# Optimization experiments

Hardware: AMD Instinct MI355X
Metric: run time of the kernel (lower is better)

## Reference

```python
import jax, jax.numpy as jnp
import numpy as np

N, H, V, K = 2048, 1024, 50304, 16
C = V // K  # tokens per POS cluster


def setup_inputs() -> dict:
    key = jax.random.key(0)
    kx, ky, kw, kl = jax.random.split(key, 4)
    x = jax.random.normal(kx, (N, H), dtype=jnp.float32)
    y = jax.random.randint(ky, (N,), 0, V, dtype=jnp.int32)
    # consistent POS label: token y belongs to cluster y // C
    y_pos = (y // C).astype(jnp.int32)
    # pos2token[i] = token ids of cluster i (equal contiguous partition)
    pos2token = jnp.arange(V, dtype=jnp.int32).reshape(K, C)
    # token_in_pos_id[i][v] = within-cluster index of token v in cluster i
    token_in_pos_id = jnp.broadcast_to(jnp.arange(V, dtype=jnp.int32) % C, (K, V))
    cluster_w = jax.random.normal(kw, (H, K), dtype=jnp.float32) * 0.02
    logits = jax.random.normal(kl, (H, V), dtype=jnp.float32) * 0.02
    return {"x": x, "y": y, "y_pos": y_pos, "pos2token": pos2token,
            "token_in_pos_id": token_in_pos_id, "cluster_w": cluster_w, "logits": logits}


def reference(x, y, y_pos, pos2token, token_in_pos_id, cluster_w, logits):
    # cluster (POS) log-probs: [N, K]
    cluster_ll = jax.nn.log_softmax(x @ cluster_w, axis=1)
    # per-cluster weight slices gathered once: [H, K, C]
    W = logits[:, pos2token.reshape(-1)].reshape(H, K, C)
    # tail logits for every token against every cluster's token set: [N, K, C]
    tail_lp = jax.nn.log_softmax(jnp.einsum('nh,hkc->nkc', x, W), axis=-1)
    n = jnp.arange(y.shape[0])
    within = token_in_pos_id[y_pos, y]          # within-cluster target id
    nll = -cluster_ll[n, y_pos] - tail_lp[n, y_pos, within]
    return nll
```

## Files before the change

kernel.cpp:

```cpp
#include <hip/hip_runtime.h>
#include <hip/hip_bf16.h>
#include <stdint.h>

#define NROW 2048
#define HDIM 1024
#define VOC  50304
#define KCL  16
#define CDIM 3144

#define MT 64
#define NT 128
#define BK 32
#define MAXTILES 48

#define WS_SUMEXP 0
#define WS_COUNTS 2048
#define WS_PART   2064
#define WS_ZTGT   4112
#define WS_TCOL   6160
#define WS_ROWS   8208
#define WS_NTILE  40976
#define WS_TILES  40977
#define WS_XB     65536
#define WS_BT     (65536 + 1048576)

typedef unsigned short u16;
typedef __attribute__((ext_vector_type(8))) short short8;
typedef __attribute__((ext_vector_type(4))) float f32x4;
typedef __attribute__((ext_vector_type(4))) unsigned short ushort4v;
typedef __attribute__((ext_vector_type(8))) unsigned short ushort8v;

__device__ __forceinline__ ushort2 f2bf2(float a, float b) {
    union { __hip_bfloat162 h; ushort2 u; } cv;
    cv.h = __float22bfloat162_rn(float2{a, b});
    return cv.u;
}

__device__ __forceinline__ void gload16(const void* g, void* lds) {
    __builtin_amdgcn_global_load_lds(
        (__attribute__((address_space(1))) void*)(g),
        (__attribute__((address_space(3))) void*)(lds), 16, 0, 0);
}

__global__ void scatter_kernel(const int* __restrict__ y,
                               const int* __restrict__ y_pos,
                               const int* __restrict__ tip,
                               int* ws_i) {
    int n = blockIdx.x * 256 + threadIdx.x;
    if (n >= NROW) return;
    int kn = y_pos[n];
    int slot = atomicAdd(&ws_i[WS_COUNTS + kn], 1);
    ws_i[WS_ROWS + kn * NROW + slot] = n;
    ws_i[WS_TCOL + n] = tip[kn * VOC + y[n]];
}

__global__ void plan_kernel(int* ws_i) {
    if (threadIdx.x == 0) {
        int t = 0;
        for (int k = 0; k < KCL; k++) {
            int mk = ws_i[WS_COUNTS + k];
            int nt = (mk + MT - 1) / MT;
            for (int r = 0; r < nt; r++) {
                ws_i[WS_TILES + 2 * t]     = k;
                ws_i[WS_TILES + 2 * t + 1] = r;
                t++;
            }
        }
        ws_i[WS_NTILE] = t;
    }
}

__global__ void cluster_kernel(const float* __restrict__ x,
                               const float* __restrict__ cw,
                               const int* __restrict__ y_pos,
                               float* ws_f) {
    int wave = threadIdx.x >> 6;
    int lane = threadIdx.x & 63;
    int n = blockIdx.x * 4 + wave;
    float acc[KCL];
#pragma unroll
    for (int k = 0; k < KCL; k++) acc[k] = 0.f;
#pragma unroll
    for (int j = 0; j < 16; j++) {
        int h = j * 64 + lane;
        float xv = x[(size_t)n * HDIM + h];
        const float4* cwr = (const float4*)(cw + (size_t)h * KCL);
#pragma unroll
        for (int q = 0; q < 4; q++) {
            float4 w = cwr[q];
            acc[q * 4 + 0] += xv * w.x;
            acc[q * 4 + 1] += xv * w.y;
            acc[q * 4 + 2] += xv * w.z;
            acc[q * 4 + 3] += xv * w.w;
        }
    }
#pragma unroll
    for (int off = 32; off >= 1; off >>= 1) {
#pragma unroll
        for (int k = 0; k < KCL; k++) acc[k] += __shfl_down(acc[k], off);
    }
    if (lane == 0) {
        int kn = y_pos[n];
        float m = acc[0];
#pragma unroll
        for (int k = 1; k < KCL; k++) m = fmaxf(m, acc[k]);
        float s = 0.f, skn = 0.f;
#pragma unroll
        for (int k = 0; k < KCL; k++) {
            s += __expf(acc[k] - m);
            skn = (k == kn) ? acc[k] : skn;
        }
        ws_f[WS_PART + n] = (m + __logf(s)) - skn;
    }
}

__global__ void convx_kernel(const float* __restrict__ x, u16* __restrict__ xb) {
    int t = blockIdx.x * 256 + threadIdx.x;
    float4 f = ((const float4*)x)[t];
    ushort2 a = f2bf2(f.x, f.y);
    ushort2 b = f2bf2(f.z, f.w);
    ushort4v v = {a.x, a.y, b.x, b.y};
    *(ushort4v*)(xb + (size_t)t * 4) = v;
}

#define TV 128
#define TH 128
#define THP 136
__global__ void transpose_kernel(const float* __restrict__ L, u16* __restrict__ Bt) {
    __shared__ u16 Ls[TV * THP];
    const int v0 = blockIdx.x * TV;
    const int h0 = blockIdx.y * TH;
    const int t  = threadIdx.x;
    {
        const int vi = (t & 31) * 4;
        const int hi = t >> 5;
#pragma unroll
        for (int p = 0; p < 16; p++) {
            int hh = p * 8 + hi;
            float4 f = *(const float4*)(L + (size_t)(h0 + hh) * VOC + v0 + vi);
            ushort2 u01 = f2bf2(f.x, f.y);
            ushort2 u23 = f2bf2(f.z, f.w);
            Ls[(vi + 0) * THP + hh] = u01.x;
            Ls[(vi + 1) * THP + hh] = u01.y;
            Ls[(vi + 2) * THP + hh] = u23.x;
            Ls[(vi + 3) * THP + hh] = u23.y;
        }
    }
    __syncthreads();
    {
        const int hi = (t & 15) * 8;
        const int vi = t >> 4;
#pragma unroll
        for (int p = 0; p < 8; p++) {
            int v = p * 16 + vi;
            ushort8v val = *(const ushort8v*)&Ls[v * THP + hi];
            *(ushort8v*)(Bt + (size_t)(v0 + v) * HDIM + h0 + hi) = val;
        }
    }
}

__launch_bounds__(256, 4)
__global__ void tail_kernel(const u16* __restrict__ xb,
                            const u16* __restrict__ Bt,
                            const int* ws_i, float* ws_f) {
    __shared__ __align__(16) u16 As[MT * BK];
    __shared__ __align__(16) u16 Bs[NT * BK];
    __shared__ int   lrow[MT];
    __shared__ int   ltcol[MT];
    __shared__ float rowsum[MT];

    const int ntile = ws_i[WS_NTILE];
    if ((int)blockIdx.y >= ntile) return;
    const int kcl = ws_i[WS_TILES + 2 * blockIdx.y];
    const int rt  = ws_i[WS_TILES + 2 * blockIdx.y + 1];
    const int ct  = blockIdx.x;
    const int Mk  = ws_i[WS_COUNTS + kcl];

    const int tid = threadIdx.x;
    if (tid < MT) {
        int r = rt * MT + tid;
        int rid = (r < Mk) ? ws_i[WS_ROWS + kcl * NROW + r] : -1;
        lrow[tid]  = rid;
        ltcol[tid] = (rid >= 0) ? ws_i[WS_TCOL + rid] : -1;
        rowsum[tid] = 0.f;
    }
    __syncthreads();

    const int w    = tid >> 6;
    const int l    = tid & 63;
    const int quad = l >> 4;
    const int lm   = l & 15;

    int arow = w * 16 + (l >> 2);
    int rid_s = lrow[arow]; if (rid_s < 0) rid_s = 0;
    const u16* agp = xb + (size_t)rid_s * HDIM + (l & 3) * 8;
    u16* alds = (u16*)As + w * 512;
    int c0 = w * 32 + (l >> 2);
    int c1 = c0 + 16;
    int g0 = ct * NT + c0; if (g0 >= CDIM) g0 = CDIM - 1;
    int g1 = ct * NT + c1; if (g1 >= CDIM) g1 = CDIM - 1;
    const u16* bgp0 = Bt + (size_t)(kcl * CDIM + g0) * HDIM + (l & 3) * 8;
    const u16* bgp1 = Bt + (size_t)(kcl * CDIM + g1) * HDIM + (l & 3) * 8;
    u16* blds0 = (u16*)Bs + w * 1024;
    u16* blds1 = (u16*)Bs + w * 1024 + 512;

    f32x4 acc[4][2];
#pragma unroll
    for (int mi = 0; mi < 4; mi++)
#pragma unroll
        for (int ni = 0; ni < 2; ni++) acc[mi][ni] = (f32x4)(0.f);

    for (int h0 = 0; h0 < HDIM; h0 += BK) {
        gload16(agp, alds);
        gload16(bgp0, blds0);
        gload16(bgp1, blds1);
        agp += BK; bgp0 += BK; bgp1 += BK;
        __syncthreads();

        short8 a[4], b[2];
#pragma unroll
        for (int mi = 0; mi < 4; mi++)
            a[mi] = *(const short8*)&As[(mi * 16 + lm) * BK + quad * 8];
#pragma unroll
        for (int ni = 0; ni < 2; ni++)
            b[ni] = *(const short8*)&Bs[(w * 32 + ni * 16 + lm) * BK + quad * 8];
#pragma unroll
        for (int mi = 0; mi < 4; mi++)
#pragma unroll
            for (int ni = 0; ni < 2; ni++)
                acc[mi][ni] = __builtin_amdgcn_mfma_f32_16x16x32_bf16(
                    a[mi], b[ni], acc[mi][ni], 0, 0, 0);
        __syncthreads();
    }

#pragma unroll
    for (int mi = 0; mi < 4; mi++) {
#pragma unroll
        for (int r = 0; r < 4; r++) {
            int row_local = mi * 16 + quad * 4 + r;
            int rid = lrow[row_local];
            int tc  = ltcol[row_local];
            float s = 0.f;
#pragma unroll
            for (int ni = 0; ni < 2; ni++) {
                int cl = ct * NT + w * 32 + ni * 16 + lm;
                float z = acc[mi][ni][r];
                if (rid >= 0 && cl < CDIM) {
                    s += __expf(z);
                    if (cl == tc) ws_f[WS_ZTGT + rid] = z;
                }
            }
            s += __shfl_xor(s, 1);
            s += __shfl_xor(s, 2);
            s += __shfl_xor(s, 4);
            s += __shfl_xor(s, 8);
            if (lm == 0 && rid >= 0) atomicAdd(&rowsum[row_local], s);
        }
    }
    __syncthreads();
    if (tid < MT) {
        int rid = lrow[tid];
        if (rid >= 0) atomicAdd(&ws_f[WS_SUMEXP + rid], rowsum[tid]);
    }
}

__global__ void finalize_kernel(const float* ws_f, float* __restrict__ out) {
    int n = blockIdx.x * 256 + threadIdx.x;
    if (n >= NROW) return;
    out[n] = ws_f[WS_PART + n] + __logf(ws_f[WS_SUMEXP + n]) - ws_f[WS_ZTGT + n];
}

extern "C" void kernel_launch(void* const* d_in, const int* in_sizes, int n_in,
                              void* d_out, int out_size, void* d_ws, size_t ws_size,
                              hipStream_t stream) {
    const float* x      = (const float*)d_in[0];
    const int*   y      = (const int*)d_in[1];
    const int*   y_pos  = (const int*)d_in[2];
    const int*   tip    = (const int*)d_in[4];
    const float* cw     = (const float*)d_in[5];
    const float* logits = (const float*)d_in[6];
    float* out  = (float*)d_out;
    float* ws_f = (float*)d_ws;
    int*   ws_i = (int*)d_ws;
    u16*   xb   = (u16*)((float*)d_ws + WS_XB);
    u16*   Bt   = (u16*)((float*)d_ws + WS_BT);

    hipMemsetAsync(d_ws, 0, (size_t)(NROW + KCL) * 4, stream);

    scatter_kernel<<<NROW / 256, 256, 0, stream>>>(y, y_pos, tip, ws_i);
    plan_kernel<<<1, 64, 0, stream>>>(ws_i);
    cluster_kernel<<<NROW / 4, 256, 0, stream>>>(x, cw, y_pos, ws_f);
    convx_kernel<<<NROW * HDIM / 4 / 256, 256, 0, stream>>>(x, xb);
    transpose_kernel<<<dim3(VOC / TV, HDIM / TH), 256, 0, stream>>>(logits, Bt);

    dim3 grid((CDIM + NT - 1) / NT, MAXTILES);
    tail_kernel<<<grid, 256, 0, stream>>>(xb, Bt, ws_i, ws_f);

    finalize_kernel<<<NROW / 256, 256, 0, stream>>>(ws_f, out);
}
```

Measured before the change: 394.8 us.

## Widen tail GEMM column tile and rework logits transpose through fp32 LDS

The tail GEMM's column tile doubles from 128 to 256. Each wave now computes a 64x64 block with 16 accumulators, which raises the ratio of MFMA work to LDS and global loads. The launch-bounds occupancy hint is dropped, so register pressure may lower occupancy. The transpose kernel now stores fp32 in LDS with padding 129 and converts to bf16 on the write-out side using 8-byte stores, instead of converting before the LDS scatter. This aims to reduce bank conflicts, at the cost of narrower global writes.

```diff
diff --git a/kernel.cpp b/kernel.cpp
--- a/kernel.cpp
+++ b/kernel.cpp
@@ -9,8 +9,9 @@
 #define CDIM 3144
 
 #define MT 64
-#define NT 128
+#define NT 256
 #define BK 32
+#define NCT 13
 #define MAXTILES 48
 
 #define WS_SUMEXP 0
@@ -28,7 +29,6 @@
 typedef __attribute__((ext_vector_type(8))) short short8;
 typedef __attribute__((ext_vector_type(4))) float f32x4;
 typedef __attribute__((ext_vector_type(4))) unsigned short ushort4v;
-typedef __attribute__((ext_vector_type(8))) unsigned short ushort8v;
 
 __device__ __forceinline__ ushort2 f2bf2(float a, float b) {
     union { __hip_bfloat162 h; ushort2 u; } cv;
@@ -123,43 +123,48 @@
     *(ushort4v*)(xb + (size_t)t * 4) = v;
 }
 
-#define TV 128
+#define TV 64
 #define TH 128
-#define THP 136
+#define THP 129
 __global__ void transpose_kernel(const float* __restrict__ L, u16* __restrict__ Bt) {
-    __shared__ u16 Ls[TV * THP];
+    __shared__ float Ls[TV * THP];
     const int v0 = blockIdx.x * TV;
     const int h0 = blockIdx.y * TH;
     const int t  = threadIdx.x;
     {
-        const int vi = (t & 31) * 4;
-        const int hi = t >> 5;
-#pragma unroll
-        for (int p = 0; p < 16; p++) {
-            int hh = p * 8 + hi;
+        const int vi  = (t & 15) * 4;
+        const int hh0 = t >> 4;
+#pragma unroll
+        for (int p = 0; p < 8; p++) {
+            int hh = hh0 + p * 16;
             float4 f = *(const float4*)(L + (size_t)(h0 + hh) * VOC + v0 + vi);
-            ushort2 u01 = f2bf2(f.x, f.y);
-            ushort2 u23 = f2bf2(f.z, f.w);
-            Ls[(vi + 0) * THP + hh] = u01.x;
-            Ls[(vi + 1) * THP + hh] = u01.y;
-            Ls[(vi + 2) * THP + hh] = u23.x;
-            Ls[(vi + 3) * THP + hh] = u23.y;
+            Ls[(vi + 0) * THP + hh] = f.x;
+            Ls[(vi + 1) * THP + hh] = f.y;
+            Ls[(vi + 2) * THP + hh] = f.z;
+            Ls[(vi + 3) * THP + hh] = f.w;
         }
     }
     __syncthreads();
     {
-        const int hi = (t & 15) * 8;
-        const int vi = t >> 4;
-#pragma unroll
-        for (int p = 0; p < 8; p++) {
-            int v = p * 16 + vi;
-            ushort8v val = *(const ushort8v*)&Ls[v * THP + hi];
-            *(ushort8v*)(Bt + (size_t)(v0 + v) * HDIM + h0 + hi) = val;
-        }
-    }
-}
-
-__launch_bounds__(256, 4)
+        const int i  = t & 15;
+        const int vq = t >> 4;
+#pragma unroll
+        for (int p = 0; p < 4; p++) {
+#pragma unroll
+            for (int q = 0; q < 2; q++) {
+                int v  = vq + p * 16;
+                int h4 = i * 4 + q * 64;
+                f32x4 f = *(const f32x4*)&Ls[v * THP + h4];
+                ushort2 a = f2bf2(f[0], f[1]);
+                ushort2 b = f2bf2(f[2], f[3]);
+                ushort4v u = {a.x, a.y, b.x, b.y};
+                *(ushort4v*)(Bt + (size_t)(v0 + v) * HDIM + h0 + h4) = u;
+            }
+        }
+    }
+}
+
+__launch_bounds__(256)
 __global__ void tail_kernel(const u16* __restrict__ xb,
                             const u16* __restrict__ Bt,
                             const int* ws_i, float* ws_f) {
@@ -191,43 +196,48 @@
     const int quad = l >> 4;
     const int lm   = l & 15;
 
-    int arow = w * 16 + (l >> 2);
-    int rid_s = lrow[arow]; if (rid_s < 0) rid_s = 0;
+    int rid_s = lrow[w * 16 + (l >> 2)];
+    if (rid_s < 0) rid_s = 0;
     const u16* agp = xb + (size_t)rid_s * HDIM + (l & 3) * 8;
-    u16* alds = (u16*)As + w * 512;
-    int c0 = w * 32 + (l >> 2);
-    int c1 = c0 + 16;
-    int g0 = ct * NT + c0; if (g0 >= CDIM) g0 = CDIM - 1;
-    int g1 = ct * NT + c1; if (g1 >= CDIM) g1 = CDIM - 1;
-    const u16* bgp0 = Bt + (size_t)(kcl * CDIM + g0) * HDIM + (l & 3) * 8;
-    const u16* bgp1 = Bt + (size_t)(kcl * CDIM + g1) * HDIM + (l & 3) * 8;
-    u16* blds0 = (u16*)Bs + w * 1024;
-    u16* blds1 = (u16*)Bs + w * 1024 + 512;
-
-    f32x4 acc[4][2];
+    char* alds = (char*)As + w * 1024;
+    const u16* bgp[4];
+    char* blds[4];
+#pragma unroll
+    for (int j = 0; j < 4; j++) {
+        int col = j * 64 + w * 16 + (l >> 2);
+        int g = ct * NT + col;
+        if (g >= CDIM) g = CDIM - 1;
+        bgp[j]  = Bt + (size_t)(kcl * CDIM + g) * HDIM + (l & 3) * 8;
+        blds[j] = (char*)Bs + j * 4096 + w * 1024;
+    }
+
+    f32x4 acc[4][4];
 #pragma unroll
     for (int mi = 0; mi < 4; mi++)
 #pragma unroll
-        for (int ni = 0; ni < 2; ni++) acc[mi][ni] = (f32x4)(0.f);
+        for (int ni = 0; ni < 4; ni++) acc[mi][ni] = (f32x4)(0.f);
 
     for (int h0 = 0; h0 < HDIM; h0 += BK) {
         gload16(agp, alds);
-        gload16(bgp0, blds0);
-        gload16(bgp1, blds1);
-        agp += BK; bgp0 += BK; bgp1 += BK;
+        agp += BK;
+#pragma unroll
+        for (int j = 0; j < 4; j++) {
+            gload16(bgp[j], blds[j]);
+            bgp[j] += BK;
+        }
         __syncthreads();
 
-        short8 a[4], b[2];
+        short8 a[4], b[4];
 #pragma unroll
         for (int mi = 0; mi < 4; mi++)
             a[mi] = *(const short8*)&As[(mi * 16 + lm) * BK + quad * 8];
 #pragma unroll
-        for (int ni = 0; ni < 2; ni++)
-            b[ni] = *(const short8*)&Bs[(w * 32 + ni * 16 + lm) * BK + quad * 8];
+        for (int ni = 0; ni < 4; ni++)
+            b[ni] = *(const short8*)&Bs[(w * 64 + ni * 16 + lm) * BK + quad * 8];
 #pragma unroll
         for (int mi = 0; mi < 4; mi++)
 #pragma unroll
-            for (int ni = 0; ni < 2; ni++)
+            for (int ni = 0; ni < 4; ni++)
                 acc[mi][ni] = __builtin_amdgcn_mfma_f32_16x16x32_bf16(
                     a[mi], b[ni], acc[mi][ni], 0, 0, 0);
         __syncthreads();
@@ -242,8 +252,8 @@
             int tc  = ltcol[row_local];
             float s = 0.f;
 #pragma unroll
-            for (int ni = 0; ni < 2; ni++) {
-                int cl = ct * NT + w * 32 + ni * 16 + lm;
+            for (int ni = 0; ni < 4; ni++) {
+                int cl = ct * NT + w * 64 + ni * 16 + lm;
                 float z = acc[mi][ni][r];
                 if (rid >= 0 && cl < CDIM) {
                     s += __expf(z);
@@ -293,7 +303,7 @@
     convx_kernel<<<NROW * HDIM / 4 / 256, 256, 0, stream>>>(x, xb);
     transpose_kernel<<<dim3(VOC / TV, HDIM / TH), 256, 0, stream>>>(logits, Bt);
 
-    dim3 grid((CDIM + NT - 1) / NT, MAXTILES);
+    dim3 grid(NCT, MAXTILES);
     tail_kernel<<<grid, 256, 0, stream>>>(xb, Bt, ws_i, ws_f);
 
     finalize_kernel<<<NROW / 256, 256, 0, stream>>>(ws_f, out);
```

Result: no change. 390.1 us (-1.2%).
